# Performance work log

Hardware: AMD Instinct MI355X
Metric: run time of the kernel (lower is better)

Reference implementation:

```python
import jax, jax.numpy as jnp
import numpy as np

N, E, HS, HBS, L, SH, RBF, T, NZ, NH = 1024, 16384, 128, 32, 5, 25, 32, 50, 10, 4
HD = HS // NH
OUT = 14  # 3x0e + 2x1e + 1x2e -> 3 + 6 + 5
_rng = np.random.default_rng(7)
# fixed Clebsch-Gordan-style coupling tensor and expansion coefficients (deterministic constants)
CG = jnp.asarray((0.1 * _rng.normal(size=(SH, SH, SH))).astype(np.float32))
EXP = jnp.asarray((0.1 * _rng.normal(size=(SH, OUT, OUT))).astype(np.float32))
_SL = [(l * l, 2 * l + 1) for l in range(5)]  # per-l (offset, size) blocks in the 25-dim rep


def _real_sh(d):
    # real spherical harmonics l=0..4 of unit vectors d [E,3] -> [E,25]
    x, y, z = d[:, 0], d[:, 1], d[:, 2]
    x2, y2, z2 = x * x, y * y, z * z
    sh = [0.282095 * jnp.ones_like(x),
          0.488603 * y, 0.488603 * z, 0.488603 * x,
          1.092548 * x * y, 1.092548 * y * z, 0.315392 * (3 * z2 - 1), 1.092548 * x * z, 0.546274 * (x2 - y2),
          0.590044 * y * (3 * x2 - y2), 2.890611 * x * y * z, 0.457046 * y * (5 * z2 - 1),
          0.373176 * z * (5 * z2 - 3), 0.457046 * x * (5 * z2 - 1), 1.445306 * z * (x2 - y2),
          0.590044 * x * (x2 - 3 * y2),
          2.503343 * x * y * (x2 - y2), 1.770131 * y * z * (3 * x2 - y2), 0.946175 * x * y * (7 * z2 - 1),
          0.669047 * y * z * (7 * z2 - 3), 0.105786 * (35 * z2 * z2 - 30 * z2 + 3),
          0.669047 * x * z * (7 * z2 - 3), 0.473087 * (x2 - y2) * (7 * z2 - 1),
          1.770131 * x * z * (x2 - 3 * y2), 0.625836 * (x2 * x2 - 6 * x2 * y2 + y2 * y2)]
    return jnp.stack(sh, axis=-1)


def _rbf(r, cutoff=12.0, alpha=0.5):
    # exponential Bernstein radial basis with cosine cutoff, [E] -> [E,RBF]
    logf = np.concatenate([[0.0], np.cumsum(np.log(np.arange(1, RBF)))])
    logbinom = jnp.asarray((logf[RBF - 1] - logf - logf[::-1]).astype(np.float32))
    k = jnp.arange(RBF, dtype=jnp.float32)
    xr = jnp.exp(-alpha * r)[:, None]
    log1mx = jnp.log1p(-xr + 1e-7)
    b = jnp.exp(logbinom[None] + k[None] * (-alpha * r[:, None]) + (RBF - 1 - k)[None] * log1mx)
    fcut = 0.5 * (jnp.cos(jnp.pi * jnp.clip(r / cutoff, 0.0, 1.0)) + 1.0)
    return b * fcut[:, None]


def _mix(feat, W):
    # per-degree channel mixing: feat [*,C,25], W [5,C,D] -> [*,D,25]
    return jnp.concatenate([jnp.einsum('ncm,cd->ndm', feat[..., o:o + s], W[l])
                            for l, (o, s) in enumerate(_SL)], axis=-1)


def _forward(z, pos, edge_index, batch, t, step, embed, temb_T, temb_H, sig_W1, sig_b1, sig_W2, sig_b2,
             rad_W1, rad_b1, rad_W2, rad_b2, rad_W3, rad_b3, mix_W, Wq, Wk, Wii, Wij, path_ii, path_ij):
    n = z.shape[0]
    e = edge_index.shape[1]
    src, dst = edge_index[0], edge_index[1]
    vec = pos[src] - pos[dst]
    r = jnp.sqrt((vec * vec).sum(-1) + 1e-12)
    dvec = vec / r[:, None]
    rbf = _rbf(r)           # [E,32]
    sh = _real_sh(dvec)     # [E,25]
    nsc = embed[z]          # [N,HS]
    cat = jnp.concatenate([nsc, jnp.tile(temb_T[t][None], (n, 1)), jnp.tile(temb_H[step][None], (n, 1))], axis=-1)
    nsc = jax.nn.relu(cat @ sig_W1 + sig_b1) @ sig_W2 + sig_b2  # sigma_embedding
    x = jnp.zeros((n, HS, SH), jnp.float32).at[:, :, 0].set(nsc)  # scalar-initialized irrep features
    for l in range(L):
        # radial MLP -> per-edge per-channel tensor-product path weights
        h = jax.nn.silu(rbf @ rad_W1[l] + rad_b1[l])
        h = jax.nn.silu(h @ rad_W2[l] + rad_b2[l])
        w = h @ rad_W3[l] + rad_b3[l]                    # [E,HS]
        Tk = jnp.einsum('ej,ijk->eik', sh, CG)           # [E,25,25] CG-coupled SH operator
        msg = jnp.einsum('eci,eik->eck', x[src], Tk) * w[:, :, None]  # per-edge TP message [E,HS,25]
        agg = jax.ops.segment_sum(msg, dst, num_segments=n)
        y = _mix(agg, mix_W[l])
        # equivariant edge attention (scalars drive logits, full irreps are values)
        q = (x[:, :, 0] @ Wq[l]).reshape(n, NH, HD)
        kk = (x[:, :, 0] @ Wk[l]).reshape(n, NH, HD)
        logits = (q[dst] * kk[src]).sum(-1) * (1.0 / float(np.sqrt(HD)))  # [E,NH]
        m = jax.ops.segment_max(logits, dst, num_segments=n)
        m = jnp.where(jnp.isfinite(m), m, 0.0)
        a = jnp.exp(logits - m[dst])
        den = jax.ops.segment_sum(a, dst, num_segments=n)
        alpha = a / (den[dst] + 1e-9)
        v = x[src].reshape(e, NH, HD, SH)
        att = jax.ops.segment_sum(alpha[:, :, None, None] * v, dst, num_segments=n).reshape(n, HS, SH)
        x = x + y + att
        # gate nonlinearity: ssp/silu on scalars, sigmoid gate on higher-l blocks
        g = jax.nn.sigmoid(x[:, :, 0:1])
        x = jnp.concatenate([jax.nn.silu(x[:, :, 0:1]), x[:, :, 1:] * g], axis=-1)
    # expansion to hamiltonian blocks (3x0e+2x1e+1x2e -> 14x14)
    fii = _mix(x, Wii)                    # [N,HBS,25]
    fij = _mix(x[src] + x[dst], Wij)      # [E,HBS,25]
    w_ii = nsc @ path_ii                  # [N,HBS] path weights
    w_ij = jnp.concatenate([nsc[src], nsc[dst]], axis=-1) @ path_ij  # [E,HBS]
    H_ii = jnp.einsum('nd,ndm,mpq->npq', w_ii, fii, EXP)  # [N,14,14]
    H_ij = jnp.einsum('ed,edm,mpq->epq', w_ij, fij, EXP)  # [E,14,14]
    return H_ii, H_ij


def setup_inputs() -> dict:
    key = jax.random.key(0)
    ks = jax.random.split(key, 40)
    def nrm(i, shape, s):
        return (jax.random.normal(ks[i], shape) * s).astype(jnp.float32)
    inp = {}
    inp['z'] = jax.random.randint(ks[0], (N,), 0, NZ)
    inp['pos'] = nrm(1, (N, 3), 3.0)
    inp['edge_index'] = jax.random.randint(ks[2], (2, E), 0, N)
    inp['batch'] = jnp.sort(jax.random.randint(ks[3], (N,), 0, 8))
    inp['t'] = 25
    inp['step'] = 10
    inp['embed'] = nrm(4, (NZ, HS), 1.0)
    inp['temb_T'] = nrm(5, (T, HS), 1.0)
    inp['temb_H'] = nrm(6, (T, HS), 1.0)
    inp['sig_W1'] = nrm(7, (3 * HS, HS), (3 * HS) ** -0.5)
    inp['sig_b1'] = jnp.zeros((HS,), jnp.float32)
    inp['sig_W2'] = nrm(8, (HS, HS), HS ** -0.5)
    inp['sig_b2'] = jnp.zeros((HS,), jnp.float32)
    inp['rad_W1'] = nrm(9, (L, RBF, 64), RBF ** -0.5)
    inp['rad_b1'] = jnp.zeros((L, 64), jnp.float32)
    inp['rad_W2'] = nrm(10, (L, 64, 64), 64 ** -0.5)
    inp['rad_b2'] = jnp.zeros((L, 64), jnp.float32)
    inp['rad_W3'] = nrm(11, (L, 64, HS), 64 ** -0.5)
    inp['rad_b3'] = jnp.zeros((L, HS), jnp.float32)
    inp['mix_W'] = nrm(12, (L, 5, HS, HS), HS ** -0.5)
    inp['Wq'] = nrm(13, (L, HS, HS), HS ** -0.5)
    inp['Wk'] = nrm(14, (L, HS, HS), HS ** -0.5)
    inp['Wii'] = nrm(15, (5, HS, HBS), HS ** -0.5)
    inp['Wij'] = nrm(16, (5, HS, HBS), HS ** -0.5)
    inp['path_ii'] = nrm(17, (HS, HBS), HS ** -0.5)
    inp['path_ij'] = nrm(18, (2 * HS, HBS), (2 * HS) ** -0.5)
    return inp


def reference(z, pos, edge_index, batch, t, step, embed, temb_T, temb_H, sig_W1, sig_b1, sig_W2, sig_b2,
              rad_W1, rad_b1, rad_W2, rad_b2, rad_W3, rad_b3, mix_W, Wq, Wk, Wii, Wij, path_ii, path_ij):
    return _forward(z, pos, edge_index, batch, t, step, embed, temb_T, temb_H, sig_W1, sig_b1, sig_W2, sig_b2,
                    rad_W1, rad_b1, rad_W2, rad_b2, rad_W3, rad_b3, mix_W, Wq, Wk, Wii, Wij, path_ii, path_ij)
```

## Files before the change

kernel.cpp:

```cpp
#include <hip/hip_runtime.h>
#include <cstdint>
#include <cmath>
#include <cstddef>

constexpr int NN   = 1024;
constexpr int NE   = 16384;
constexpr int HSZ  = 128;
constexpr int NSH  = 25;
constexpr int NRBF = 32;
constexpr int NLAY = 5;
constexpr int XSZ  = HSZ * NSH;
constexpr int HII_SZ = NN * 196;
constexpr int TKP  = 800;


constexpr size_t OFF_CONSTS = 0;
constexpr size_t OFF_X    = 20560;
constexpr size_t OFF_AGG  = OFF_X    + (size_t)NN * XSZ;
constexpr size_t OFF_ATT  = OFF_AGG  + (size_t)NN * XSZ;
constexpr size_t OFF_X0   = OFF_ATT  + (size_t)NN * XSZ;
constexpr size_t OFF_NSC  = OFF_X0   + (size_t)NN * HSZ;
constexpr size_t OFF_Q    = OFF_NSC  + (size_t)NN * HSZ;
constexpr size_t OFF_K    = OFF_Q    + (size_t)NN * HSZ;
constexpr size_t OFF_RBF  = OFF_K    + (size_t)NN * HSZ;
constexpr size_t OFF_SH   = OFF_RBF  + (size_t)NE * NRBF;
constexpr size_t OFF_TK   = OFF_SH   + (size_t)NE * NSH;
constexpr size_t OFF_WRAD = OFF_TK   + (size_t)NE * TKP;
constexpr size_t OFF_INT  = OFF_WRAD + (size_t)NE * HSZ;
constexpr size_t NEED_BYTES = OFF_INT * 4 + (size_t)(1024 + 1025 + 1024 + 16384) * 4;

namespace qhc {

struct Pcg64 {
  unsigned __int128 state, inc;
  static unsigned __int128 mult() {
    return (((unsigned __int128)2549297995355413924ULL) << 64) | 4865540595714422341ULL;
  }
  void step() { state = state * mult() + inc; }
  uint64_t next64() {
    step();
    uint64_t hi = (uint64_t)(state >> 64), lo = (uint64_t)state;
    uint64_t x = hi ^ lo;
    unsigned rot = (unsigned)(state >> 122);
    return (x >> rot) | (x << ((64u - rot) & 63u));
  }
  double nextd() { return (double)(next64() >> 11) * (1.0 / 9007199254740992.0); }
};

struct HostConsts {
  float buf[20560];
  HostConsts() {
    const uint32_t INIT_A = 0x43b0d7e5u, MULT_A = 0x931e8875u;
    const uint32_t INIT_B = 0x8b51f9ddu, MULT_B = 0x58f38dedu;
    uint32_t pool[4];
    uint32_t hc = INIT_A;
    auto hashf = [&](uint32_t v) -> uint32_t {
      v ^= hc; hc *= MULT_A; v *= hc; v ^= v >> 16; return v;
    };
    auto mixf = [](uint32_t x, uint32_t y) -> uint32_t {
      uint32_t r = x * 0xca01f9ddu - y * 0x4973f715u;
      r ^= r >> 16;
      return r;
    };
    pool[0] = hashf(7u);
    for (int i = 1; i < 4; i++) pool[i] = hashf(0u);
    for (int s = 0; s < 4; s++)
      for (int d = 0; d < 4; d++)
        if (s != d) pool[d] = mixf(pool[d], hashf(pool[s]));
    uint32_t st32[8];
    uint32_t hb = INIT_B;
    for (int i = 0; i < 8; i++) {
      uint32_t v = pool[i % 4];
      v ^= hb; hb *= MULT_B; v *= hb; v ^= v >> 16;
      st32[i] = v;
    }
    uint64_t w0 = st32[0] | ((uint64_t)st32[1] << 32);
    uint64_t w1 = st32[2] | ((uint64_t)st32[3] << 32);
    uint64_t w2 = st32[4] | ((uint64_t)st32[5] << 32);
    uint64_t w3 = st32[6] | ((uint64_t)st32[7] << 32);
    unsigned __int128 seed = (((unsigned __int128)w0) << 64) | w1;
    unsigned __int128 incs = (((unsigned __int128)w2) << 64) | w3;
    Pcg64 g;
    g.state = 0; g.inc = (incs << 1) | 1;
    g.step(); g.state += seed; g.step();
    double wi[256], fi[256]; uint64_t ki[256];
    {
      const double m1 = 4503599627370496.0;
      double dn = 3.6541528853610087963519472518, tn = dn, vn = 0.00492867323399941;
      double q = vn / std::exp(-0.5 * dn * dn);
      ki[0] = (uint64_t)((dn / q) * m1); ki[1] = 0;
      wi[0] = q / m1; wi[255] = dn / m1;
      fi[0] = 1.0; fi[255] = std::exp(-0.5 * dn * dn);
      for (int i = 254; i >= 1; i--) {
        dn = std::sqrt(-2.0 * std::log(vn / dn + std::exp(-0.5 * dn * dn)));
        ki[i + 1] = (uint64_t)((dn / tn) * m1);
        tn = dn;
        fi[i] = std::exp(-0.5 * dn * dn);
        wi[i] = dn / m1;
      }
    }
    const double ZR = 3.6541528853610087963519472518;
    const double ZIR = 0.27366123732975827203338247596;
    auto stdnorm = [&]() -> double {
      for (;;) {
        uint64_t r = g.next64();
        int idx = (int)(r & 0xff);
        r >>= 8;
        int sign = (int)(r & 1);
        uint64_t rabs = (r >> 1) & 0x000fffffffffffffULL;
        double xv = (double)rabs * wi[idx];
        if (sign) xv = -xv;
        if (rabs < ki[idx]) return xv;
        if (idx == 0) {
          for (;;) {
            double xx = -ZIR * std::log1p(-g.nextd());
            double yy = -std::log1p(-g.nextd());
            if (yy + yy > xx * xx)
              return ((rabs >> 8) & 1) ? -(ZR + xx) : (ZR + xx);
          }
        } else {
          if (((fi[idx - 1] - fi[idx]) * g.nextd() + fi[idx]) < std::exp(-0.5 * xv * xv))
            return xv;
        }
      }
    };
    for (int i = 0; i < 15625 + 4900; i++) buf[i] = (float)(0.1 * stdnorm());
    double logf[32]; logf[0] = 0.0;
    for (int i = 1; i < 32; i++) logf[i] = logf[i - 1] + std::log((double)i);
    for (int k = 0; k < 32; k++) buf[15625 + 4900 + k] = (float)(logf[31] - logf[k] - logf[31 - k]);
    buf[20557] = buf[20558] = buf[20559] = 0.f;
  }
};
static HostConsts g_hc;
}

__device__ __forceinline__ float siluf(float a) { return a / (1.f + expf(-a)); }

__global__ __launch_bounds__(256) void qh_geom(
    const float* __restrict__ pos, const int* __restrict__ ei,
    const float* __restrict__ lbn, float* __restrict__ rbf, float* __restrict__ sh) {
  int e = blockIdx.x * 256 + threadIdx.x;
  if (e >= NE) return;
  int s = ei[e], d = ei[NE + e];
  float vx = pos[s * 3 + 0] - pos[d * 3 + 0];
  float vy = pos[s * 3 + 1] - pos[d * 3 + 1];
  float vz = pos[s * 3 + 2] - pos[d * 3 + 2];
  float r = sqrtf(vx * vx + vy * vy + vz * vz + 1e-12f);
  float inv = 1.0f / r;
  float x = vx * inv, y = vy * inv, z = vz * inv;
  float x2 = x * x, y2 = y * y, z2 = z * z;
  float* sp = sh + (size_t)e * NSH;
  sp[0] = 0.282095f;
  sp[1] = 0.488603f * y;
  sp[2] = 0.488603f * z;
  sp[3] = 0.488603f * x;
  sp[4] = 1.092548f * x * y;
  sp[5] = 1.092548f * y * z;
  sp[6] = 0.315392f * (3.f * z2 - 1.f);
  sp[7] = 1.092548f * x * z;
  sp[8] = 0.546274f * (x2 - y2);
  sp[9] = 0.590044f * y * (3.f * x2 - y2);
  sp[10] = 2.890611f * x * y * z;
  sp[11] = 0.457046f * y * (5.f * z2 - 1.f);
  sp[12] = 0.373176f * z * (5.f * z2 - 3.f);
  sp[13] = 0.457046f * x * (5.f * z2 - 1.f);
  sp[14] = 1.445306f * z * (x2 - y2);
  sp[15] = 0.590044f * x * (x2 - 3.f * y2);
  sp[16] = 2.503343f * x * y * (x2 - y2);
  sp[17] = 1.770131f * y * z * (3.f * x2 - y2);
  sp[18] = 0.946175f * x * y * (7.f * z2 - 1.f);
  sp[19] = 0.669047f * y * z * (7.f * z2 - 3.f);
  sp[20] = 0.105786f * (35.f * z2 * z2 - 30.f * z2 + 3.f);
  sp[21] = 0.669047f * x * z * (7.f * z2 - 3.f);
  sp[22] = 0.473087f * (x2 - y2) * (7.f * z2 - 1.f);
  sp[23] = 1.770131f * x * z * (x2 - 3.f * y2);
  sp[24] = 0.625836f * (x2 * x2 - 6.f * x2 * y2 + y2 * y2);
  float xr = expf(-0.5f * r);
  float l1 = log1pf(-xr + 1e-7f);
  float fc = 0.5f * (cosf(3.14159265358979323846f * fminf(r * (1.0f / 12.0f), 1.0f)) + 1.0f);
  float* rp = rbf + (size_t)e * NRBF;
  for (int k = 0; k < NRBF; k++) {
    float b = expf(lbn[k] + (float)k * (-0.5f * r) + (float)(NRBF - 1 - k) * l1);
    rp[k] = b * fc;
  }
}

__global__ __launch_bounds__(256) void qh_tk(
    const float* __restrict__ sh, const float* __restrict__ CG, float* __restrict__ Tkp) {
  __shared__ float shl[32 * NSH];
  int e0 = blockIdx.x * 32;
  int t = threadIdx.x;
  for (int i = t; i < 32 * NSH; i += 256) shl[i] = sh[(size_t)e0 * NSH + i];
  for (int i = t; i < 32 * TKP; i += 256) Tkp[(size_t)e0 * TKP + i] = 0.f;
  __syncthreads();
  for (int ik = t; ik < NSH * NSH; ik += 256) {
    int i = ik / NSH, k = ik % NSH;
    int pos = i * 32 + k + (k >= 7) + 2 * (k >= 13) + 2 * (k >= 19);
    float cg[NSH];
#pragma unroll
    for (int j = 0; j < NSH; j++) cg[j] = CG[i * 625 + j * NSH + k];
    for (int ee = 0; ee < 32; ee++) {
      float acc = 0.f;
#pragma unroll
      for (int j = 0; j < NSH; j++) acc += shl[ee * NSH + j] * cg[j];
      Tkp[(size_t)(e0 + ee) * TKP + pos] = acc;
    }
  }
}

__global__ __launch_bounds__(128) void qh_nsc(
    const int* __restrict__ z, const int* __restrict__ tptr, const int* __restrict__ sptr,
    const float* __restrict__ embed, const float* __restrict__ tT, const float* __restrict__ tH,
    const float* __restrict__ W1, const float* __restrict__ b1,
    const float* __restrict__ W2, const float* __restrict__ b2,
    float* __restrict__ nsc, float* __restrict__ x, float* __restrict__ x0) {
  __shared__ float cat[384];
  __shared__ float h[128];
  int nd = blockIdx.x, d = threadIdx.x;
  int zz = z[nd], tt = tptr[0], st = sptr[0];
  cat[d] = embed[zz * HSZ + d];
  cat[128 + d] = tT[tt * HSZ + d];
  cat[256 + d] = tH[st * HSZ + d];
  __syncthreads();
  float a = b1[d];
  for (int c = 0; c < 384; c++) a += cat[c] * W1[c * HSZ + d];
  h[d] = fmaxf(a, 0.f);
  __syncthreads();
  a = b2[d];
  for (int c = 0; c < 128; c++) a += h[c] * W2[c * HSZ + d];
  nsc[nd * HSZ + d] = a;
  x0[nd * HSZ + d] = a;
  float* xr = x + (size_t)nd * XSZ + d;
  xr[0] = a;
  for (int m = 1; m < NSH; m++) xr[m * 128] = 0.f;
}

__global__ __launch_bounds__(256) void qh_zero(int* counts) {
  int i = blockIdx.x * 256 + threadIdx.x;
  if (i < NN) counts[i] = 0;
}
__global__ __launch_bounds__(256) void qh_count(const int* __restrict__ ei, int* counts) {
  int e = blockIdx.x * 256 + threadIdx.x;
  if (e < NE) atomicAdd(&counts[ei[NE + e]], 1);
}
__global__ __launch_bounds__(1024) void qh_scan(const int* __restrict__ counts,
                                                int* starts, int* cursor) {
  __shared__ int tmp[NN];
  int t = threadIdx.x;
  tmp[t] = counts[t];
  __syncthreads();
  for (int ofs = 1; ofs < NN; ofs <<= 1) {
    int v = (t >= ofs) ? tmp[t - ofs] : 0;
    __syncthreads();
    tmp[t] += v;
    __syncthreads();
  }
  starts[t + 1] = tmp[t];
  if (t == 0) starts[0] = 0;
  cursor[t] = (t == 0) ? 0 : tmp[t - 1];
}
__global__ __launch_bounds__(256) void qh_scatter(const int* __restrict__ ei,
                                                  int* cursor, int* perm) {
  int e = blockIdx.x * 256 + threadIdx.x;
  if (e < NE) {
    int d = ei[NE + e];
    int pos = atomicAdd(&cursor[d], 1);
    perm[pos] = e;
  }
}

__global__ __launch_bounds__(256) void qh_rad(
    const float* __restrict__ rbf,
    const float* __restrict__ W1, const float* __restrict__ b1,
    const float* __restrict__ W2, const float* __restrict__ b2,
    const float* __restrict__ W3, const float* __restrict__ b3,
    float* __restrict__ wrad) {
  __shared__ float w1l[2048], w2l[4096], w3l[8192];
  __shared__ float rl[4][32], h1[4][64], h2[4][64];
  int t = threadIdx.x;
  for (int i = t; i < 2048; i += 256) w1l[i] = W1[i];
  for (int i = t; i < 4096; i += 256) w2l[i] = W2[i];
  for (int i = t; i < 8192; i += 256) w3l[i] = W3[i];
  __syncthreads();
  int e0 = blockIdx.x * 16;
  for (int q = 0; q < 4; q++) {
    int eb = e0 + q * 4;
    if (t < 128) rl[t >> 5][t & 31] = rbf[(size_t)(eb + (t >> 5)) * NRBF + (t & 31)];
    __syncthreads();
    {
      int eg = t >> 6, u = t & 63;
      float a = b1[u];
      for (int c = 0; c < 32; c++) a += rl[eg][c] * w1l[c * 64 + u];
      h1[eg][u] = siluf(a);
    }
    __syncthreads();
    {
      int eg = t >> 6, u = t & 63;
      float a = b2[u];
      for (int c = 0; c < 64; c++) a += h1[eg][c] * w2l[c * 64 + u];
      h2[eg][u] = siluf(a);
    }
    __syncthreads();
#pragma unroll
    for (int p = 0; p < 2; p++) {
      int eg = (t >> 7) + p * 2, u = t & 127;
      float a = b3[u];
      for (int c = 0; c < 64; c++) a += h2[eg][c] * w3l[c * 128 + u];
      wrad[(size_t)(eb + eg) * HSZ + u] = a;
    }
    __syncthreads();
  }
}

__global__ __launch_bounds__(256) void qh_qk(
    const float* __restrict__ x0, const float* __restrict__ Wq, const float* __restrict__ Wk,
    float* __restrict__ q, float* __restrict__ kk) {
  __shared__ float xl[128];
  int nd = blockIdx.x, t = threadIdx.x;
  if (t < 128) xl[t] = x0[nd * HSZ + t];
  __syncthreads();
  int d = t & 127;
  const float* W = (t < 128) ? Wq : Wk;
  float a = 0.f;
  for (int c = 0; c < 128; c++) a += xl[c] * W[c * HSZ + d];
  if (t < 128) q[nd * HSZ + d] = a;
  else kk[nd * HSZ + d] = a;
}

__global__ __launch_bounds__(256) void qh_logit(
    const float* __restrict__ q, const float* __restrict__ kk,
    const int* __restrict__ ei, float* __restrict__ logits) {
  int t = threadIdx.x;
  int e = blockIdx.x * 2 + (t >> 7);
  int c = t & 127;
  int s = ei[e], d = ei[NE + e];
  float p = q[d * HSZ + c] * kk[s * HSZ + c];
#pragma unroll
  for (int m = 16; m >= 1; m >>= 1) p += __shfl_xor(p, m);
  if ((c & 31) == 0) logits[e * 4 + (c >> 5)] = p * 0.17677669529663687f;
}

__global__ __launch_bounds__(64) void qh_soft(
    const float* __restrict__ logits, const int* __restrict__ starts,
    const int* __restrict__ perm, float* __restrict__ alpha) {
  int nd = blockIdx.x, t = threadIdx.x;
  int hh = t >> 4, l = t & 15;
  int jb = starts[nd], je = starts[nd + 1];
  float m = -1e30f;
  for (int j = jb + l; j < je; j += 16) m = fmaxf(m, logits[perm[j] * 4 + hh]);
#pragma unroll
  for (int s = 1; s < 16; s <<= 1) m = fmaxf(m, __shfl_xor(m, s));
  float den = 0.f;
  for (int j = jb + l; j < je; j += 16) den += expf(logits[perm[j] * 4 + hh] - m);
#pragma unroll
  for (int s = 1; s < 16; s <<= 1) den += __shfl_xor(den, s);
  float inv = 1.f / (den + 1e-9f);
  for (int j = jb + l; j < je; j += 16) {
    int e = perm[j];
    alpha[e * 4 + hh] = expf(logits[e * 4 + hh] - m) * inv;
  }
}

__global__ __launch_bounds__(256, 8) void qh_msgatt(
    const float* __restrict__ x, const float* __restrict__ Tkp,
    const float* __restrict__ wrad, const float* __restrict__ alpha,
    const int* __restrict__ starts, const int* __restrict__ perm,
    const int* __restrict__ ei,
    float* __restrict__ agg, float* __restrict__ att) {
  __shared__ __align__(16) float xs[2][1600];
  __shared__ float wl[2][64];
  int bid = blockIdx.x;
  int nd = (bid >> 4) * 8 + (bid & 7);
  int h  = (bid >> 3) & 1;
  int t = threadIdx.x;
  int cl = t & 63, q4 = t >> 6;
  int q4u = __builtin_amdgcn_readfirstlane(q4);
  int c = h * 64 + cl;
  int k0 = (q4 == 0) ? 0 : (1 + 6 * q4);
  int nk = (q4 == 0) ? 7 : 6;
  float am[7], aa[7];
#pragma unroll
  for (int u = 0; u < 7; u++) { am[u] = 0.f; aa[u] = 0.f; }
  int jb = starts[nd], je = starts[nd + 1];

  float4 rxA = {0, 0, 0, 0}, rxB = {0, 0, 0, 0};
  float rw = 0.f;
  if (jb < je) {
    int e = perm[jb], s = ei[e];
    const float* xb0 = x + (size_t)s * XSZ + h * 64;
    rxA = *(const float4*)(xb0 + (t >> 4) * 128 + (t & 15) * 4);
    if (t < 144) rxB = *(const float4*)(xb0 + ((256 + t) >> 4) * 128 + (t & 15) * 4);
    if (t < 64) rw = wrad[(size_t)e * HSZ + h * 64 + t];
    ((float4*)xs[0])[t] = rxA;
    if (t < 144) ((float4*)xs[0])[256 + t] = rxB;
    if (t < 64) wl[0][t] = rw;
  }
  __syncthreads();
  for (int j = jb; j < je; j++) {
    int cur = (j - jb) & 1, nxt = cur ^ 1;
    int e = perm[j];
    int eu = __builtin_amdgcn_readfirstlane(e);
    const float* tkr = Tkp + (size_t)eu * TKP + q4u * 8;
    float al = alpha[e * 4 + (c >> 5)];
    bool more = (j + 1 < je);
    if (more) {
      int e2 = perm[j + 1], s2 = ei[e2];
      const float* xb2 = x + (size_t)s2 * XSZ + h * 64;
      rxA = *(const float4*)(xb2 + (t >> 4) * 128 + (t & 15) * 4);
      if (t < 144) rxB = *(const float4*)(xb2 + ((256 + t) >> 4) * 128 + (t & 15) * 4);
      if (t < 64) rw = wrad[(size_t)e2 * HSZ + h * 64 + t];
    }
    float wc = wl[cur][cl];
#pragma unroll 5
    for (int i = 0; i < NSH; i++) {
      float xw = xs[cur][i * 64 + cl] * wc;
      float4 t0 = *(const float4*)(tkr + i * 32);
      float4 t1 = *(const float4*)(tkr + i * 32 + 4);
      am[0] += xw * t0.x; am[1] += xw * t0.y; am[2] += xw * t0.z; am[3] += xw * t0.w;
      am[4] += xw * t1.x; am[5] += xw * t1.y; am[6] += xw * t1.z;
    }
#pragma unroll
    for (int u = 0; u < 7; u++)
      if (u < nk) aa[u] += al * xs[cur][(k0 + u) * 64 + cl];
    __syncthreads();
    if (more) {
      ((float4*)xs[nxt])[t] = rxA;
      if (t < 144) ((float4*)xs[nxt])[256 + t] = rxB;
      if (t < 64) wl[nxt][t] = rw;
    }
    __syncthreads();
  }
#pragma unroll
  for (int u = 0; u < 7; u++)
    if (u < nk) {
      agg[(size_t)nd * XSZ + (k0 + u) * 128 + c] = am[u];
      att[(size_t)nd * XSZ + (k0 + u) * 128 + c] = aa[u];
    }
}

__global__ __launch_bounds__(256) void qh_mixgemm(
    const float* __restrict__ mixW, float* __restrict__ agg) {
  __shared__ __align__(16) float Wl[16384];
  __shared__ __align__(16) float Al[4096];
  int b = blockIdx.x, t = threadIdx.x;
  int lb, cum;
  if (b < 32)       { lb = 0; cum = 0; }
  else if (b < 128) { lb = 1; cum = 32; }
  else if (b < 288) { lb = 2; cum = 128; }
  else if (b < 512) { lb = 3; cum = 288; }
  else              { lb = 4; cum = 512; }
  int sl = 2 * lb + 1, o = lb * lb;
  int row0 = (b - cum) * 32;
  const float* W = mixW + lb * 16384;
  for (int i = t; i < 1024; i += 256) {
    int r = i >> 5, c4 = (i & 31) * 4;
    int gr = row0 + r, n = gr / sl, m = o + gr - n * sl;
    *(float4*)&Al[r * 128 + c4] =
        *(const float4*)&agg[(size_t)n * XSZ + m * 128 + c4];
  }
  for (int i = t; i < 4096; i += 256)
    *(float4*)&Wl[i * 4] = *(const float4*)&W[i * 4];
  __syncthreads();
  int d4 = (t & 31) * 4;
  int rg = t >> 5;
  float acc[4][4];
#pragma unroll
  for (int r = 0; r < 4; r++)
#pragma unroll
    for (int q = 0; q < 4; q++) acc[r][q] = 0.f;
  for (int cc = 0; cc < 128; cc++) {
    float4 w4 = *(const float4*)&Wl[cc * 128 + d4];
#pragma unroll
    for (int r = 0; r < 4; r++) {
      float a = Al[(rg * 4 + r) * 128 + cc];
      acc[r][0] += a * w4.x; acc[r][1] += a * w4.y;
      acc[r][2] += a * w4.z; acc[r][3] += a * w4.w;
    }
  }
#pragma unroll
  for (int r = 0; r < 4; r++) {
    int gr = row0 + rg * 4 + r, n = gr / sl, m = o + gr - n * sl;
    float4 v; v.x = acc[r][0]; v.y = acc[r][1]; v.z = acc[r][2]; v.w = acc[r][3];
    *(float4*)&agg[(size_t)n * XSZ + m * 128 + d4] = v;
  }
}

__global__ __launch_bounds__(256) void qh_gate(
    const float* __restrict__ y, const float* __restrict__ att,
    float* __restrict__ x, float* __restrict__ x0) {
  __shared__ float v0l[128];
  int nd = blockIdx.x, t = threadIdx.x;
  int d = t & 127, mh = t >> 7;
  int m0 = mh ? 13 : 0, nm = mh ? 12 : 13;
  float v[13];
  size_t base = (size_t)nd * XSZ + (size_t)m0 * 128 + d;
#pragma unroll
  for (int u = 0; u < 13; u++)
    if (u < nm) v[u] = x[base + (size_t)u * 128] + y[base + (size_t)u * 128] + att[base + (size_t)u * 128];
  if (mh == 0) v0l[d] = v[0];
  __syncthreads();
  float g = 1.f / (1.f + expf(-v0l[d]));
#pragma unroll
  for (int u = 0; u < 13; u++)
    if (u < nm) x[base + (size_t)u * 128] = v[u] * g;
  if (mh == 0) x0[nd * HSZ + d] = v[0] * g;
}

__global__ __launch_bounds__(256) void qh_prep(
    const float* __restrict__ x, const float* __restrict__ nsc,
    const float* __restrict__ Wii, const float* __restrict__ Wij,
    const float* __restrict__ pii, const float* __restrict__ pij,
    const float* __restrict__ EXPc,
    float* __restrict__ fm, float* __restrict__ awb, float* __restrict__ out) {
  __shared__ float xl[XSZ];
  __shared__ float nl[128];
  __shared__ float wc[4096];
  __shared__ float fml[800];
  __shared__ float wiil[32];
  __shared__ float gl[25];
  int nd = blockIdx.x, t = threadIdx.x;
  for (int i = t; i < XSZ; i += 256) xl[i] = x[(size_t)nd * XSZ + i];
  if (t < 128) nl[t] = nsc[nd * HSZ + t];
  __syncthreads();
  if (t < 32) {
    float a = 0.f;
    for (int cc = 0; cc < 128; cc++) a += nl[cc] * pii[cc * 32 + t];
    wiil[t] = a;
  } else if (t < 96) {
    int d = (t - 32) & 31;
    int half = (t - 32) >> 5;
    const float* pp = pij + (half ? 128 * 32 : 0);
    float a = 0.f;
    for (int cc = 0; cc < 128; cc++) a += nl[cc] * pp[cc * 32 + d];
    awb[nd * 64 + half * 32 + d] = a;
  }
  for (int lb = 0; lb < 5; lb++) {
    __syncthreads();
    for (int i = t; i < 4096; i += 256) wc[i] = Wii[lb * 4096 + i];
    __syncthreads();
    int o = lb * lb, sl = 2 * lb + 1;
    for (int idx = t; idx < 32 * sl; idx += 256) {
      int d = idx & 31, m = o + (idx >> 5);
      float a = 0.f;
      for (int cc = 0; cc < 128; cc++) a += xl[m * 128 + cc] * wc[cc * 32 + d];
      fml[d * NSH + m] = a;
    }
  }
  __syncthreads();
  if (t < 25) {
    float a = 0.f;
#pragma unroll
    for (int d = 0; d < 32; d++) a += wiil[d] * fml[d * NSH + t];
    gl[t] = a;
  }
  __syncthreads();
  if (t < 196) {
    float a = 0.f;
#pragma unroll
    for (int m = 0; m < 25; m++) a += gl[m] * EXPc[m * 196 + t];
    out[(size_t)nd * 196 + t] = a;
  }
  for (int lb = 0; lb < 5; lb++) {
    __syncthreads();
    for (int i = t; i < 4096; i += 256) wc[i] = Wij[lb * 4096 + i];
    __syncthreads();
    int o = lb * lb, sl = 2 * lb + 1;
    for (int idx = t; idx < 32 * sl; idx += 256) {
      int d = idx & 31, m = o + (idx >> 5);
      float a = 0.f;
      for (int cc = 0; cc < 128; cc++) a += xl[m * 128 + cc] * wc[cc * 32 + d];
      fm[(size_t)nd * 800 + d * NSH + m] = a;
    }
  }
}

__global__ __launch_bounds__(256) void qh_fij2(
    const int* __restrict__ ei, const float* __restrict__ fm,
    const float* __restrict__ awb, const float* __restrict__ EXPc,
    float* __restrict__ out) {
  __shared__ float fsum[800], wsum[32], gl[25];
  int e = blockIdx.x, t = threadIdx.x;
  int s = ei[e], d2 = ei[NE + e];
  for (int i = t; i < 800; i += 256)
    fsum[i] = fm[(size_t)s * 800 + i] + fm[(size_t)d2 * 800 + i];
  if (t < 32) wsum[t] = awb[s * 64 + t] + awb[d2 * 64 + 32 + t];
  __syncthreads();
  if (t < 25) {
    float a = 0.f;
#pragma unroll
    for (int d = 0; d < 32; d++) a += wsum[d] * fsum[d * NSH + t];
    gl[t] = a;
  }
  __syncthreads();
  if (t < 196) {
    float a = 0.f;
#pragma unroll
    for (int m = 0; m < 25; m++) a += gl[m] * EXPc[m * 196 + t];
    out[HII_SZ + (size_t)e * 196 + t] = a;
  }
}

extern "C" void kernel_launch(void* const* d_in, const int* in_sizes, int n_in,
                              void* d_out, int out_size, void* d_ws, size_t ws_size,
                              hipStream_t stream) {
  (void)in_sizes; (void)n_in; (void)out_size;
  if (ws_size < NEED_BYTES) return;

  const int*   z    = (const int*)d_in[0];
  const float* pos  = (const float*)d_in[1];
  const int*   ei   = (const int*)d_in[2];
  const int*   tptr = (const int*)d_in[4];
  const int*   sptr = (const int*)d_in[5];
  const float* embed= (const float*)d_in[6];
  const float* tT   = (const float*)d_in[7];
  const float* tH   = (const float*)d_in[8];
  const float* sW1  = (const float*)d_in[9];
  const float* sb1  = (const float*)d_in[10];
  const float* sW2  = (const float*)d_in[11];
  const float* sb2  = (const float*)d_in[12];
  const float* rW1  = (const float*)d_in[13];
  const float* rb1  = (const float*)d_in[14];
  const float* rW2  = (const float*)d_in[15];
  const float* rb2  = (const float*)d_in[16];
  const float* rW3  = (const float*)d_in[17];
  const float* rb3  = (const float*)d_in[18];
  const float* mixW = (const float*)d_in[19];
  const float* Wq   = (const float*)d_in[20];
  const float* Wk   = (const float*)d_in[21];
  const float* Wii  = (const float*)d_in[22];
  const float* Wij  = (const float*)d_in[23];
  const float* pii  = (const float*)d_in[24];
  const float* pij  = (const float*)d_in[25];

  float* ws = (float*)d_ws;
  float* CGd   = ws + OFF_CONSTS;
  float* EXPd  = CGd + 15625;
  float* LBNd  = CGd + 15625 + 4900;
  float* x     = ws + OFF_X;
  float* agg   = ws + OFF_AGG;
  float* att   = ws + OFF_ATT;
  float* x0    = ws + OFF_X0;
  float* nsc   = ws + OFF_NSC;
  float* qarr  = ws + OFF_Q;
  float* karr  = ws + OFF_K;
  float* rbf   = ws + OFF_RBF;
  float* sh    = ws + OFF_SH;
  float* Tkp   = ws + OFF_TK;
  float* wrad  = ws + OFF_WRAD;
  float* logits = ws + OFF_SH;
  float* alphaA = ws + OFF_SH + 65536;
  float* fm     = ws + OFF_AGG;
  float* awb    = ws + OFF_AGG + 819200;
  int* ibase   = (int*)(ws + OFF_INT);
  int* counts  = ibase;
  int* starts  = ibase + 1024;
  int* cursor  = ibase + 1024 + 1025;
  int* perm    = ibase + 1024 + 1025 + 1024;
  float* outp  = (float*)d_out;

  hipMemcpyAsync(CGd, qhc::g_hc.buf, 20557 * sizeof(float), hipMemcpyHostToDevice, stream);

  qh_geom<<<NE / 256, 256, 0, stream>>>(pos, ei, LBNd, rbf, sh);
  qh_tk<<<NE / 32, 256, 0, stream>>>(sh, CGd, Tkp);
  qh_nsc<<<NN, 128, 0, stream>>>(z, tptr, sptr, embed, tT, tH, sW1, sb1, sW2, sb2, nsc, x, x0);
  qh_zero<<<NN / 256, 256, 0, stream>>>(counts);
  qh_count<<<NE / 256, 256, 0, stream>>>(ei, counts);
  qh_scan<<<1, 1024, 0, stream>>>(counts, starts, cursor);
  qh_scatter<<<NE / 256, 256, 0, stream>>>(ei, cursor, perm);

  for (int l = 0; l < NLAY; l++) {
    qh_rad<<<NE / 16, 256, 0, stream>>>(rbf,
        rW1 + (size_t)l * 32 * 64, rb1 + (size_t)l * 64,
        rW2 + (size_t)l * 64 * 64, rb2 + (size_t)l * 64,
        rW3 + (size_t)l * 64 * 128, rb3 + (size_t)l * 128, wrad);
    qh_qk<<<NN, 256, 0, stream>>>(x0, Wq + (size_t)l * 16384, Wk + (size_t)l * 16384, qarr, karr);
    qh_logit<<<NE / 2, 256, 0, stream>>>(qarr, karr, ei, logits);
    qh_soft<<<NN, 64, 0, stream>>>(logits, starts, perm, alphaA);
    qh_msgatt<<<NN * 2, 256, 0, stream>>>(x, Tkp, wrad, alphaA, starts, perm, ei, agg, att);
    qh_mixgemm<<<800, 256, 0, stream>>>(mixW + (size_t)l * 81920, agg);
    qh_gate<<<NN, 256, 0, stream>>>(agg, att, x, x0);
  }

  qh_prep<<<NN, 256, 0, stream>>>(x, nsc, Wii, Wij, pii, pij, EXPd, fm, awb, outp);
  qh_fij2<<<NE, 256, 0, stream>>>(ei, fm, awb, EXPd, outp);
}
```

Measured before the change: 1.208 ms.

## Split per-node edge loop in message kernel across two blocks with partial buffers

The message/attention kernel now launches twice as many blocks. Each node's incoming edge range is split in half, and each half writes its partial agg/att sums to a separate buffer. The mix GEMM sums the two agg partials when loading, and the gate kernel adds the second att partial. This is meant to raise parallelism and shorten the serial per-node edge chain, which is long at about 16 edges per node. The cost is extra workspace, extra global writes and reads of partial buffers, and a second pipeline warm-up per block.

```diff
diff --git a/kernel.cpp b/kernel.cpp
--- a/kernel.cpp
+++ b/kernel.cpp
@@ -26,7 +26,9 @@
 constexpr size_t OFF_SH   = OFF_RBF  + (size_t)NE * NRBF;
 constexpr size_t OFF_TK   = OFF_SH   + (size_t)NE * NSH;
 constexpr size_t OFF_WRAD = OFF_TK   + (size_t)NE * TKP;
-constexpr size_t OFF_INT  = OFF_WRAD + (size_t)NE * HSZ;
+constexpr size_t OFF_AGG2 = OFF_WRAD + (size_t)NE * HSZ;
+constexpr size_t OFF_ATT2 = OFF_AGG2 + (size_t)NN * XSZ;
+constexpr size_t OFF_INT  = OFF_ATT2 + (size_t)NN * XSZ;
 constexpr size_t NEED_BYTES = OFF_INT * 4 + (size_t)(1024 + 1025 + 1024 + 16384) * 4;
 
 namespace qhc {
@@ -366,12 +368,14 @@
     const float* __restrict__ wrad, const float* __restrict__ alpha,
     const int* __restrict__ starts, const int* __restrict__ perm,
     const int* __restrict__ ei,
-    float* __restrict__ agg, float* __restrict__ att) {
+    float* __restrict__ agg, float* __restrict__ att,
+    float* __restrict__ agg2, float* __restrict__ att2) {
   __shared__ __align__(16) float xs[2][1600];
   __shared__ float wl[2][64];
   int bid = blockIdx.x;
-  int nd = (bid >> 4) * 8 + (bid & 7);
+  int nd = (bid >> 5) * 8 + (bid & 7);
   int h  = (bid >> 3) & 1;
+  int ch = (bid >> 4) & 1;
   int t = threadIdx.x;
   int cl = t & 63, q4 = t >> 6;
   int q4u = __builtin_amdgcn_readfirstlane(q4);
@@ -382,11 +386,15 @@
 #pragma unroll
   for (int u = 0; u < 7; u++) { am[u] = 0.f; aa[u] = 0.f; }
   int jb = starts[nd], je = starts[nd + 1];
+  int cnt = je - jb;
+  int half1 = (cnt + 1) >> 1;
+  int cb = ch ? (jb + half1) : jb;
+  int ce = ch ? je : (jb + half1);
 
   float4 rxA = {0, 0, 0, 0}, rxB = {0, 0, 0, 0};
   float rw = 0.f;
-  if (jb < je) {
-    int e = perm[jb], s = ei[e];
+  if (cb < ce) {
+    int e = perm[cb], s = ei[e];
     const float* xb0 = x + (size_t)s * XSZ + h * 64;
     rxA = *(const float4*)(xb0 + (t >> 4) * 128 + (t & 15) * 4);
     if (t < 144) rxB = *(const float4*)(xb0 + ((256 + t) >> 4) * 128 + (t & 15) * 4);
@@ -396,13 +404,13 @@
     if (t < 64) wl[0][t] = rw;
   }
   __syncthreads();
-  for (int j = jb; j < je; j++) {
-    int cur = (j - jb) & 1, nxt = cur ^ 1;
+  for (int j = cb; j < ce; j++) {
+    int cur = (j - cb) & 1, nxt = cur ^ 1;
     int e = perm[j];
     int eu = __builtin_amdgcn_readfirstlane(e);
     const float* tkr = Tkp + (size_t)eu * TKP + q4u * 8;
     float al = alpha[e * 4 + (c >> 5)];
-    bool more = (j + 1 < je);
+    bool more = (j + 1 < ce);
     if (more) {
       int e2 = perm[j + 1], s2 = ei[e2];
       const float* xb2 = x + (size_t)s2 * XSZ + h * 64;
@@ -430,16 +438,19 @@
     }
     __syncthreads();
   }
+  float* ga = ch ? agg2 : agg;
+  float* ta = ch ? att2 : att;
 #pragma unroll
   for (int u = 0; u < 7; u++)
     if (u < nk) {
-      agg[(size_t)nd * XSZ + (k0 + u) * 128 + c] = am[u];
-      att[(size_t)nd * XSZ + (k0 + u) * 128 + c] = aa[u];
+      ga[(size_t)nd * XSZ + (k0 + u) * 128 + c] = am[u];
+      ta[(size_t)nd * XSZ + (k0 + u) * 128 + c] = aa[u];
     }
 }
 
 __global__ __launch_bounds__(256) void qh_mixgemm(
-    const float* __restrict__ mixW, float* __restrict__ agg) {
+    const float* __restrict__ mixW, float* __restrict__ agg,
+    const float* __restrict__ agg2) {
   __shared__ __align__(16) float Wl[16384];
   __shared__ __align__(16) float Al[4096];
   int b = blockIdx.x, t = threadIdx.x;
@@ -455,8 +466,11 @@
   for (int i = t; i < 1024; i += 256) {
     int r = i >> 5, c4 = (i & 31) * 4;
     int gr = row0 + r, n = gr / sl, m = o + gr - n * sl;
-    *(float4*)&Al[r * 128 + c4] =
-        *(const float4*)&agg[(size_t)n * XSZ + m * 128 + c4];
+    size_t idx = (size_t)n * XSZ + m * 128 + c4;
+    float4 a = *(const float4*)&agg[idx];
+    float4 b4 = *(const float4*)&agg2[idx];
+    float4 v; v.x = a.x + b4.x; v.y = a.y + b4.y; v.z = a.z + b4.z; v.w = a.w + b4.w;
+    *(float4*)&Al[r * 128 + c4] = v;
   }
   for (int i = t; i < 4096; i += 256)
     *(float4*)&Wl[i * 4] = *(const float4*)&W[i * 4];
@@ -487,6 +501,7 @@
 
 __global__ __launch_bounds__(256) void qh_gate(
     const float* __restrict__ y, const float* __restrict__ att,
+    const float* __restrict__ att2,
     float* __restrict__ x, float* __restrict__ x0) {
   __shared__ float v0l[128];
   int nd = blockIdx.x, t = threadIdx.x;
@@ -496,7 +511,8 @@
   size_t base = (size_t)nd * XSZ + (size_t)m0 * 128 + d;
 #pragma unroll
   for (int u = 0; u < 13; u++)
-    if (u < nm) v[u] = x[base + (size_t)u * 128] + y[base + (size_t)u * 128] + att[base + (size_t)u * 128];
+    if (u < nm) v[u] = x[base + (size_t)u * 128] + y[base + (size_t)u * 128]
+                     + att[base + (size_t)u * 128] + att2[base + (size_t)u * 128];
   if (mh == 0) v0l[d] = v[0];
   __syncthreads();
   float g = 1.f / (1.f + expf(-v0l[d]));
@@ -647,6 +663,8 @@
   float* sh    = ws + OFF_SH;
   float* Tkp   = ws + OFF_TK;
   float* wrad  = ws + OFF_WRAD;
+  float* agg2  = ws + OFF_AGG2;
+  float* att2  = ws + OFF_ATT2;
   float* logits = ws + OFF_SH;
   float* alphaA = ws + OFF_SH + 65536;
   float* fm     = ws + OFF_AGG;
@@ -676,9 +694,10 @@
     qh_qk<<<NN, 256, 0, stream>>>(x0, Wq + (size_t)l * 16384, Wk + (size_t)l * 16384, qarr, karr);
     qh_logit<<<NE / 2, 256, 0, stream>>>(qarr, karr, ei, logits);
     qh_soft<<<NN, 64, 0, stream>>>(logits, starts, perm, alphaA);
-    qh_msgatt<<<NN * 2, 256, 0, stream>>>(x, Tkp, wrad, alphaA, starts, perm, ei, agg, att);
-    qh_mixgemm<<<800, 256, 0, stream>>>(mixW + (size_t)l * 81920, agg);
-    qh_gate<<<NN, 256, 0, stream>>>(agg, att, x, x0);
+    qh_msgatt<<<NN * 4, 256, 0, stream>>>(x, Tkp, wrad, alphaA, starts, perm, ei,
+                                          agg, att, agg2, att2);
+    qh_mixgemm<<<800, 256, 0, stream>>>(mixW + (size_t)l * 81920, agg, agg2);
+    qh_gate<<<NN, 256, 0, stream>>>(agg, att, att2, x, x0);
   }
 
   qh_prep<<<NN, 256, 0, stream>>>(x, nsc, Wii, Wij, pii, pij, EXPd, fm, awb, outp);
```

After: 1.589 ms. 31.6% more time.
